# Performance work log

Measured on AMD Instinct MI355X. Metric: run time of the kernel, lower is better.

## Reference

```python
import jax, jax.numpy as jnp
import numpy as np

SAMPLE_POINTS = 1000
THRESH = 0.1
MAX_RATIO = 0.1
BIG = 1e9


def _sobel_boundary(mask):
    # mask: [B, H, W] -> boundary magnitude [B, H, W]
    kx = jnp.array([[-1, 0, 1], [-2, 0, 2], [-1, 0, 1]], jnp.float32).reshape(1, 1, 3, 3)
    ky = jnp.array([[-1, -2, -1], [0, 0, 0], [1, 2, 1]], jnp.float32).reshape(1, 1, 3, 3)
    x = mask[:, None, :, :]
    dn = ('NCHW', 'OIHW', 'NCHW')
    gx = jax.lax.conv_general_dilated(x, kx, (1, 1), [(1, 1), (1, 1)], dimension_numbers=dn)
    gy = jax.lax.conv_general_dilated(x, ky, (1, 1), [(1, 1), (1, 1)], dimension_numbers=dn)
    return jnp.sqrt(gx * gx + gy * gy + 1e-8)[:, 0]


def _extract_points(bmap, keys, H, W):
    # bmap: [B, H, W]. Returns points [B, P, 2] float and validity mask [B, P].
    # Torch version uses torch.where + randperm subsampling; here we pick a
    # uniformly-random subset of valid boundary pixels via noisy top_k
    # (fixed-shape, jit-compatible stream compaction).
    def one(bm, key):
        flat = bm.reshape(-1)
        valid = flat > THRESH
        noise = jax.random.uniform(key, flat.shape)
        score = valid.astype(jnp.float32) * 2.0 + noise  # valid in (2,3), invalid in (0,1)
        _, idx = jax.lax.top_k(score, SAMPLE_POINTS)
        pts = jnp.stack([(idx // W).astype(jnp.float32), (idx % W).astype(jnp.float32)], axis=-1)
        pvalid = valid[idx]
        has_any = valid.any()
        # empty-boundary fallback: single center point (like torch version)
        center = jnp.array([H // 2, W // 2], jnp.float32)
        pts = jnp.where(has_any, pts, jnp.broadcast_to(center, pts.shape))
        pvalid = jnp.where(has_any, pvalid, jnp.arange(SAMPLE_POINTS) == 0)
        return pts, pvalid

    return jax.vmap(one)(bmap, keys)


def _hausdorff(pp, pv, tp, tv, diag):
    # pp: [B,P,2], tp: [B,T,2]; masked symmetric Hausdorff per batch element.
    pp2 = jnp.sum(pp * pp, -1)  # [B,P]
    tp2 = jnp.sum(tp * tp, -1)  # [B,T]
    d2 = pp2[:, :, None] + tp2[:, None, :] - 2.0 * jnp.einsum('bpc,btc->bpt', pp, tp)
    D = jnp.sqrt(jnp.maximum(d2, 0.0))  # [B,P,T]
    min_p2t = jnp.min(jnp.where(tv[:, None, :], D, BIG), axis=2)  # [B,P]
    a = jnp.max(jnp.where(pv, min_p2t, -BIG), axis=1)  # [B]
    min_t2p = jnp.min(jnp.where(pv[:, :, None], D, BIG), axis=1)  # [B,T]
    b = jnp.max(jnp.where(tv, min_t2p, -BIG), axis=1)  # [B]
    hd = jnp.maximum(a, b) / diag
    return jnp.clip(hd, 0.0, MAX_RATIO)


def setup_inputs() -> dict:
    key = jax.random.key(0)
    k1, k2 = jax.random.split(key)
    B, H, W = 64, 512, 512
    pred_logits = jax.random.normal(k1, (B, H, W), dtype=jnp.float32)
    target = (jax.random.uniform(k2, (B, H, W)) > 0.5).astype(jnp.float32)
    return {"pred_logits": pred_logits, "target": target}


def reference(pred_logits, target):
    B, H, W = pred_logits.shape
    pred_probs = jax.nn.sigmoid(pred_logits)
    bmap_pred = _sobel_boundary(pred_probs)
    bmap_tgt = _sobel_boundary(target)
    keys = jax.random.split(jax.random.key(1), 2 * B)
    pp, pv = _extract_points(bmap_pred, keys[:B], H, W)
    tp, tv = _extract_points(bmap_tgt, keys[B:], H, W)
    diag = jnp.sqrt(jnp.float32(H * H + W * W))
    hd = _hausdorff(pp, pv, tp, tv, diag)  # [B]
    return jnp.mean(hd)
```

## Files before the change

kernel.cpp:

```cpp
#include <hip/hip_runtime.h>
#include <stdint.h>


#define HH 512
#define WW 512
#define NPIX (HH * WW)
#define NSEL 1000
#define SLICE_CAP 320
#define CUTM (253u << 14)
#define BITCUT ((((253u << 15) - 1u)) << 9)
#define ROWS_PER 32
#define K2_BS 1024

#if __has_builtin(__builtin_amdgcn_alignbit)
__device__ __forceinline__ uint32_t rotl32(uint32_t x, int r) {
  return __builtin_amdgcn_alignbit(x, x, (32 - r) & 31);
}
#else
__device__ __forceinline__ uint32_t rotl32(uint32_t x, int r) {
  return (x << r) | (x >> (32 - r));
}
#endif

template <int R>
__device__ __forceinline__ uint32_t rotlT(uint32_t x) {
  uint32_t d;
  asm("v_alignbit_b32 %0, %1, %1, %2" : "=v"(d) : "v"(x), "n"(32 - R));
  return d;
}

__device__ __forceinline__ void tf2x32(uint32_t k0, uint32_t k1,
                                       uint32_t c0, uint32_t c1,
                                       uint32_t& o0, uint32_t& o1) {
  uint32_t ks2 = k0 ^ k1 ^ 0x1BD11BDAu;
  uint32_t x0 = c0 + k0, x1 = c1 + k1;
#define TF_R(r) { x0 += x1; x1 = rotl32(x1, (r)); x1 ^= x0; }
  TF_R(13) TF_R(15) TF_R(26) TF_R(6)
  x0 += k1;  x1 += ks2 + 1u;
  TF_R(17) TF_R(29) TF_R(16) TF_R(24)
  x0 += ks2; x1 += k0 + 2u;
  TF_R(13) TF_R(15) TF_R(26) TF_R(6)
  x0 += k0;  x1 += k1 + 3u;
  TF_R(17) TF_R(29) TF_R(16) TF_R(24)
  x0 += k1;  x1 += ks2 + 4u;
  TF_R(13) TF_R(15) TF_R(26) TF_R(6)
  x0 += ks2; x1 += k0 + 5u;
#undef TF_R
  o0 = x0; o1 = x1;
}

__device__ __forceinline__ uint32_t m_from_bits(uint32_t bits) {
  float noise = __uint_as_float((bits >> 9) | 0x3F800000u) - 1.0f;
  float score = 2.0f + noise;
  return __float_as_uint(score) - 0x40000000u;
}

__device__ __forceinline__ uint32_t pixel_m(uint32_t k0, uint32_t k1, int p) {
  uint32_t b1, b2;
  tf2x32(k0, k1, 0u, (uint32_t)p, b1, b2);
  return m_from_bits(b1 ^ b2);
}

__device__ __forceinline__ float sigf(float x) { return 1.0f / (1.0f + __expf(-x)); }

__device__ __forceinline__ float ldval(const float* __restrict__ img, int r, int c, bool isPred) {
  if (r < 0 || r > HH - 1 || c < 0 || c > WW - 1) return 0.0f;
  float v = img[(size_t)r * WW + c];
  return isPred ? sigf(v) : v;
}

__device__ __forceinline__ uint32_t pack_pt(uint32_t p) {
  return ((p >> 9) << 16) | (p & 511u);
}

template <bool PRED>
__device__ __forceinline__ void sobel_body(const float* __restrict__ img, int b,
                                           int slice, int t,
                                           unsigned long long* stage, int* s_cn,
                                           int* s_cv) {
  const int lane = t & 63, w = t >> 6;
  const int rbase = slice * ROWS_PER + 8 * w;
  uint32_t k0, k1;
  tf2x32(0u, 1u, 0u, (uint32_t)b, k0, k1);
  k0 = __builtin_amdgcn_readfirstlane(k0);
  k1 = __builtin_amdgcn_readfirstlane(k1);
  const uint32_t ks2 = k0 ^ k1 ^ 0x1BD11BDAu;

  float P[10], Q[10], R[10];
  float4 na, nb;
  int cnt = 0;
  const uint32_t pbase = (uint32_t)((rbase << 9) + (lane << 3));

  auto issue = [&](int rn) {
    if ((unsigned)rn < (unsigned)HH) {
      const float* rp = img + ((size_t)rn << 9) + (lane << 3);
      na = *(const float4*)rp;
      nb = *(const float4*)(rp + 4);
    }
  };
  auto promote = [&](float (&vv)[10], int rn) {
    if ((unsigned)rn < (unsigned)HH) {
      float4 x = na, y = nb;
      if (PRED) {
        x.x = sigf(x.x); x.y = sigf(x.y); x.z = sigf(x.z); x.w = sigf(x.w);
        y.x = sigf(y.x); y.y = sigf(y.y); y.z = sigf(y.z); y.w = sigf(y.w);
      }
      vv[1] = x.x; vv[2] = x.y; vv[3] = x.z; vv[4] = x.w;
      vv[5] = y.x; vv[6] = y.y; vv[7] = y.z; vv[8] = y.w;
      float l = __shfl_up(y.w, 1);
      float r = __shfl_down(x.x, 1);
      vv[0] = (lane == 0) ? 0.0f : l;
      vv[9] = (lane == 63) ? 0.0f : r;
    } else {
#pragma unroll
      for (int i = 0; i < 10; ++i) vv[i] = 0.0f;
    }
  };

  issue(rbase - 1); promote(P, rbase - 1);
  issue(rbase);     promote(Q, rbase);
  issue(rbase + 1);

#pragma unroll 1
  for (int r = 0; r < 8; ++r) {
    promote(R, rbase + r + 1);
    if (r < 7) issue(rbase + r + 2);
    __builtin_amdgcn_sched_barrier(0);

    const uint32_t prow = pbase + ((uint32_t)r << 9);
    uint32_t X0[8], X1[8];
    const uint32_t pk = prow + k1;
    const uint32_t s0 = pk + k0;
#pragma unroll
    for (int j = 0; j < 8; ++j) {
      uint32_t x1i = pk + (uint32_t)j;
      X0[j] = s0 + (uint32_t)j;
      X1[j] = rotlT<13>(x1i) ^ X0[j];
    }
#define RND(rr)                                                         \
  _Pragma("unroll") for (int j = 0; j < 8; ++j) {                       \
    X0[j] += X1[j];                                                     \
    X1[j] = rotlT<(rr)>(X1[j]) ^ X0[j];                                 \
  }
#define INJ(ka, kb, i)                                                  \
  _Pragma("unroll") for (int j = 0; j < 8; ++j) {                       \
    X0[j] += (ka);                                                      \
    X1[j] += (kb) + (uint32_t)(i);                                      \
  }
    RND(15) RND(26) RND(6)  INJ(k1, ks2, 1)
    RND(17) RND(29) RND(16) RND(24) INJ(ks2, k0, 2)
    RND(13) RND(15) RND(26) RND(6)  INJ(k0, k1, 3)
    RND(17) RND(29) RND(16) RND(24) INJ(k1, ks2, 4)
    RND(13) RND(15) RND(26) RND(6)  INJ(ks2, k0, 5)
#undef RND
#undef INJ
    uint32_t bits[8];
#pragma unroll
    for (int j = 0; j < 8; ++j) bits[j] = X0[j] ^ X1[j];

    float da[10], e[10];
#pragma unroll
    for (int k = 0; k < 10; ++k) {
      da[k] = R[k] - P[k];
      e[k] = P[k] + 2.0f * Q[k] + R[k];
    }
    uint32_t candmask = 0;
#pragma unroll
    for (int j = 0; j < 8; ++j) {
      float gx = e[j + 2] - e[j];
      float gy = da[j] + 2.0f * da[j + 1] + da[j + 2];
      bool vld = (gx * gx + gy * gy + 1e-8f) > 0.01f;
      cnt += vld ? 1 : 0;
      candmask |= ((vld && bits[j] >= BITCUT) ? 1u : 0u) << j;
    }
    if (candmask) {
      int base = atomicAdd(s_cn, __popc(candmask));
      do {
        int j = __ffs(candmask) - 1;
        candmask &= candmask - 1;
        if (base < SLICE_CAP) {
          uint32_t m = m_from_bits(bits[j]);
          stage[base] = ((unsigned long long)m << 32) | (prow + (uint32_t)j);
        }
        ++base;
      } while (candmask);
    }
#pragma unroll
    for (int k = 0; k < 10; ++k) { P[k] = Q[k]; Q[k] = R[k]; }
  }
#pragma unroll
  for (int o = 32; o > 0; o >>= 1) cnt += __shfl_down(cnt, o);
  if (lane == 0) atomicAdd(s_cv, cnt);
}

__global__ __launch_bounds__(256, 4) void sobel_cand(
    const float* __restrict__ pred, const float* __restrict__ tgt,
    int2* __restrict__ g_scnt, unsigned long long* __restrict__ g_cand,
    uint32_t* __restrict__ g_hmax, int* __restrict__ g_done) {
  const int bid = blockIdx.x;
  const int b = bid >> 4, s = bid & 15;
  const int t = threadIdx.x;
  __shared__ unsigned long long stage[SLICE_CAP];
  __shared__ int s_cn, s_cv;
  if (t == 0) { s_cn = 0; s_cv = 0; }
  if (bid == 0) {
    if (t < 64) g_hmax[t] = 0u;
    if (t == 64) *g_done = 0;
  }
  __syncthreads();
  if (b < 64) sobel_body<true>(pred + (size_t)b * NPIX, b, s, t, stage, &s_cn, &s_cv);
  else        sobel_body<false>(tgt + (size_t)(b - 64) * NPIX, b, s, t, stage, &s_cn, &s_cv);
  __syncthreads();
  const int raw = s_cn;
  const int n = raw < SLICE_CAP ? raw : SLICE_CAP;
  for (int i = t; i < n; i += 256) g_cand[(size_t)bid * SLICE_CAP + i] = stage[i];
  if (t == 0) g_scnt[bid] = make_int2(s_cv, raw);
}

__global__ __launch_bounds__(K2_BS) void resolve_kernel(
    const float* __restrict__ pred, const float* __restrict__ tgt,
    const int2* __restrict__ g_scnt, unsigned long long* __restrict__ g_cand,
    uint32_t* __restrict__ g_pts, int* __restrict__ g_counts) {
  const int img = blockIdx.x;
  const int t = threadIdx.x;
  const int lane = t & 63;

  __shared__ unsigned long long cand_s[16 * SLICE_CAP];
  __shared__ int segc[16], segoff[17];
  __shared__ int s_scx[16], s_scy[16];
  __shared__ int s_info[4];
  __shared__ int ch[256];
  __shared__ int fh[1024];
  __shared__ int aux[256];
  __shared__ unsigned long long ties[256];
  __shared__ int s_pos, s_nt, s_T1, s_r1, s_T2, s_r2, s_n;

  if (t < 16) {
    int2 v = g_scnt[img * 16 + t];
    s_scx[t] = v.x; s_scy[t] = v.y;
    segc[t] = v.y < SLICE_CAP ? v.y : SLICE_CAP;
  }
  if (t == 0) { s_pos = 0; s_nt = 0; }
  __syncthreads();
  if (t == 0) {
    int cv = 0, hi = 0, ovf = 0, off = 0;
    for (int s = 0; s < 16; ++s) {
      cv += s_scx[s]; hi += s_scy[s];
      if (s_scy[s] > SLICE_CAP) ovf = 1;
      segoff[s] = off; off += segc[s];
    }
    segoff[16] = off;
    s_n = off;
    s_info[0] = cv; s_info[1] = hi; s_info[2] = ovf;
  }
  __syncthreads();
  const int cv = s_info[0];
  if (cv == 0) {
    if (t == 0) { g_pts[img * NSEL] = (256u << 16) | 256u; g_counts[img] = 1; }
    return;
  }
  const int need = cv < NSEL ? cv : NSEL;
  const bool slow = (s_info[2] != 0) || (s_info[1] < need);

  unsigned long long* C = g_cand + (size_t)img * 16 * SLICE_CAP;

  if (slow) {
    const bool isPred = img < 64;
    const float* im = isPred ? pred + (size_t)img * NPIX : tgt + (size_t)(img - 64) * NPIX;
    uint32_t k0, k1;
    tf2x32(0u, 1u, 0u, (uint32_t)img, k0, k1);
    if (t < 256) ch[t] = 0;
    __syncthreads();
    for (int p = t; p < NPIX; p += K2_BS) {
      int r = p >> 9, c = p & 511;
      float gx = (ldval(im, r - 1, c + 1, isPred) - ldval(im, r - 1, c - 1, isPred)) +
                 2.0f * (ldval(im, r, c + 1, isPred) - ldval(im, r, c - 1, isPred)) +
                 (ldval(im, r + 1, c + 1, isPred) - ldval(im, r + 1, c - 1, isPred));
      float gy = (ldval(im, r + 1, c - 1, isPred) - ldval(im, r - 1, c - 1, isPred)) +
                 2.0f * (ldval(im, r + 1, c, isPred) - ldval(im, r - 1, c, isPred)) +
                 (ldval(im, r + 1, c + 1, isPred) - ldval(im, r - 1, c + 1, isPred));
      if ((gx * gx + gy * gy + 1e-8f) > 0.01f) {
        uint32_t m = pixel_m(k0, k1, p);
        uint32_t cb = m >> 14; if (cb > 255u) cb = 255u;
        atomicAdd(&ch[cb], 1);
      }
    }
    __syncthreads();
    if (t < 256) aux[t] = ch[t];
    __syncthreads();
    for (int o = 1; o < 256; o <<= 1) {
      int v = 0;
      if (t < 256 && t + o < 256) v = aux[t + o];
      __syncthreads();
      if (t < 256) aux[t] += v;
      __syncthreads();
    }
    if (t < 256) {
      int nx = (t + 1 < 256) ? aux[t + 1] : 0;
      if (aux[t] >= need && nx < need) s_T1 = t;
    }
    __syncthreads();
    const uint32_t Tc = (uint32_t)s_T1;
    if (t == 0) s_info[3] = 0;
    __syncthreads();
    for (int p = t; p < NPIX; p += K2_BS) {
      int r = p >> 9, c = p & 511;
      float gx = (ldval(im, r - 1, c + 1, isPred) - ldval(im, r - 1, c - 1, isPred)) +
                 2.0f * (ldval(im, r, c + 1, isPred) - ldval(im, r, c - 1, isPred)) +
                 (ldval(im, r + 1, c + 1, isPred) - ldval(im, r + 1, c - 1, isPred));
      float gy = (ldval(im, r + 1, c - 1, isPred) - ldval(im, r - 1, c - 1, isPred)) +
                 2.0f * (ldval(im, r + 1, c, isPred) - ldval(im, r - 1, c, isPred)) +
                 (ldval(im, r + 1, c + 1, isPred) - ldval(im, r - 1, c + 1, isPred));
      if ((gx * gx + gy * gy + 1e-8f) > 0.01f) {
        uint32_t m = pixel_m(k0, k1, p);
        uint32_t cb = m >> 14; if (cb > 255u) cb = 255u;
        if (cb >= Tc) {
          int i = atomicAdd(&s_info[3], 1);
          if (i < 16 * SLICE_CAP) C[i] = ((unsigned long long)m << 32) | (uint32_t)p;
        }
      }
    }
    __syncthreads();
    if (t == 0) s_n = s_info[3] < 16 * SLICE_CAP ? s_info[3] : 16 * SLICE_CAP;
    __syncthreads();
  }

  {
    const int nn = s_n;
    if (slow) {
      for (int i = t; i < nn; i += K2_BS) cand_s[i] = C[i];
    } else {
      for (int i = t; i < 16 * SLICE_CAP; i += K2_BS) {
        int s = i / SLICE_CAP;
        int o = i - s * SLICE_CAP;
        if (o < segc[s]) cand_s[segoff[s] + o] = C[i];
      }
    }
  }
  if (t < 256) ch[t] = 0;
  fh[t] = 0;
  __syncthreads();
  const int n = s_n;

  if (!slow) {
    int l0 = 0, l1 = 0, l2 = 0;
    for (int i = t; i < n; i += K2_BS) {
      uint32_t cb = (uint32_t)(cand_s[i] >> 32) >> 14; if (cb > 255u) cb = 255u;
      if (cb == 253u) ++l0; else if (cb == 254u) ++l1; else ++l2;
    }
#pragma unroll
    for (int o = 32; o > 0; o >>= 1) {
      l0 += __shfl_down(l0, o); l1 += __shfl_down(l1, o); l2 += __shfl_down(l2, o);
    }
    if (lane == 0) {
      if (l0) atomicAdd(&ch[253], l0);
      if (l1) atomicAdd(&ch[254], l1);
      if (l2) atomicAdd(&ch[255], l2);
    }
  } else {
    for (int i = t; i < n; i += K2_BS) {
      uint32_t cb = (uint32_t)(cand_s[i] >> 32) >> 14; if (cb > 255u) cb = 255u;
      atomicAdd(&ch[cb], 1);
    }
  }
  __syncthreads();
  if (t < 256) aux[t] = ch[t];
  __syncthreads();
  for (int o = 1; o < 256; o <<= 1) {
    int v = 0;
    if (t < 256 && t + o < 256) v = aux[t + o];
    __syncthreads();
    if (t < 256) aux[t] += v;
    __syncthreads();
  }
  if (t < 256) {
    int nx = (t + 1 < 256) ? aux[t + 1] : 0;
    if (aux[t] >= need && nx < need) { s_T1 = t; s_r1 = need - nx; }
  }
  __syncthreads();
  const uint32_t T1 = (uint32_t)s_T1;
  const int r1 = s_r1;
  const uint32_t baseM = T1 << 14;

  for (int base = 0; base < n; base += K2_BS) {
    const int i = base + t;
    const bool in = i < n;
    unsigned long long e = in ? cand_s[i] : 0ull;
    uint32_t m = (uint32_t)(e >> 32), p = (uint32_t)e;
    uint32_t cb = m >> 14; if (cb > 255u) cb = 255u;
    bool emit = in && cb > T1;
    unsigned long long msk = __ballot(emit);
    if (msk) {
      int leader = __ffsll(msk) - 1;
      int bpos = 0;
      if (lane == leader) bpos = atomicAdd(&s_pos, __popcll(msk));
      bpos = __shfl(bpos, leader);
      if (emit)
        g_pts[img * NSEL + bpos + __popcll(msk & ((1ull << lane) - 1ull))] = pack_pt(p);
    }
    if (in && cb == T1) {
      uint32_t f = (m - baseM) >> 4; if (f > 1023u) f = 1023u;
      atomicAdd(&fh[f], 1);
    }
  }
  __syncthreads();
  for (int o = 1; o < 1024; o <<= 1) {
    int v = (t + o < 1024) ? fh[t + o] : 0;
    __syncthreads();
    fh[t] += v;
    __syncthreads();
  }
  {
    int nx = (t < 1023) ? fh[t + 1] : 0;
    if (fh[t] >= r1 && nx < r1) { s_T2 = t; s_r2 = r1 - nx; }
  }
  __syncthreads();
  const int T2 = s_T2, r2 = s_r2;

  for (int base = 0; base < n; base += K2_BS) {
    const int i = base + t;
    const bool in = i < n;
    unsigned long long e = in ? cand_s[i] : 0ull;
    uint32_t m = (uint32_t)(e >> 32), p = (uint32_t)e;
    uint32_t cb = m >> 14; if (cb > 255u) cb = 255u;
    uint32_t f = (m - baseM) >> 4; if (f > 1023u) f = 1023u;
    const bool isT1 = in && cb == T1;
    bool emit = isT1 && (int)f > T2;
    bool tie  = isT1 && (int)f == T2;
    unsigned long long msk = __ballot(emit);
    if (msk) {
      int leader = __ffsll(msk) - 1;
      int bpos = 0;
      if (lane == leader) bpos = atomicAdd(&s_pos, __popcll(msk));
      bpos = __shfl(bpos, leader);
      if (emit)
        g_pts[img * NSEL + bpos + __popcll(msk & ((1ull << lane) - 1ull))] = pack_pt(p);
    }
    unsigned long long mt = __ballot(tie);
    if (mt) {
      int leader = __ffsll(mt) - 1;
      int bpos = 0;
      if (lane == leader) bpos = atomicAdd(&s_nt, __popcll(mt));
      bpos = __shfl(bpos, leader);
      int idx = bpos + __popcll(mt & ((1ull << lane) - 1ull));
      if (tie && idx < 256) ties[idx] = e;
    }
  }
  __syncthreads();
  const int nt = s_nt < 256 ? s_nt : 256;
  for (int i = t; i < nt; i += K2_BS) {
    unsigned long long e = ties[i];
    uint32_t mi = (uint32_t)(e >> 32), pi = (uint32_t)e;
    int rank = 0;
    for (int j = 0; j < nt; ++j) {
      unsigned long long e2 = ties[j];
      uint32_t mj = (uint32_t)(e2 >> 32), pj = (uint32_t)e2;
      rank += (mj > mi) || (mj == mi && pj < pi);
    }
    if (rank < r2) {
      int pos = atomicAdd(&s_pos, 1);
      g_pts[img * NSEL + pos] = pack_pt(pi);
    }
  }
  __syncthreads();
  if (t == 0) g_counts[img] = s_pos;
}

__global__ __launch_bounds__(256) void haus_kernel(
    const uint32_t* __restrict__ g_pts, const int* __restrict__ g_counts,
    uint32_t* __restrict__ g_hmax, int* __restrict__ g_done,
    float* __restrict__ out) {
  const int bid = blockIdx.x;
  const int img = bid >> 3;
  const int dir = (bid >> 2) & 1;
  const int seg = bid & 3;
  const int t = threadIdx.x;
  const int iOwn = dir ? 64 + img : img;
  const int iOth = dir ? img : 64 + img;
  const int nOwn = g_counts[iOwn];
  const int nOth = g_counts[iOth];
  __shared__ float2 o[NSEL];
  __shared__ float red[256];
  __shared__ int s_ticket;
  for (int i = t; i < nOth; i += 256) {
    uint32_t v = g_pts[iOth * NSEL + i];
    o[i] = make_float2((float)(v >> 16), (float)(v & 0xFFFFu));
  }
  __syncthreads();
  float best = 0.0f;
  const int lo = seg * 250;
  const int hi = min(nOwn, lo + 250);
  for (int i = lo + t; i < hi; i += 256) {
    uint32_t v = g_pts[iOwn * NSEL + i];
    float pr = (float)(v >> 16), pc = (float)(v & 0xFFFFu);
    float mn0 = 3.4e38f, mn1 = 3.4e38f, mn2 = 3.4e38f, mn3 = 3.4e38f;
    int j = 0;
    for (; j + 3 < nOth; j += 4) {
      float dr0 = pr - o[j].x,     dc0 = pc - o[j].y;
      float dr1 = pr - o[j + 1].x, dc1 = pc - o[j + 1].y;
      float dr2 = pr - o[j + 2].x, dc2 = pc - o[j + 2].y;
      float dr3 = pr - o[j + 3].x, dc3 = pc - o[j + 3].y;
      mn0 = fminf(mn0, dr0 * dr0 + dc0 * dc0);
      mn1 = fminf(mn1, dr1 * dr1 + dc1 * dc1);
      mn2 = fminf(mn2, dr2 * dr2 + dc2 * dc2);
      mn3 = fminf(mn3, dr3 * dr3 + dc3 * dc3);
    }
    for (; j < nOth; ++j) {
      float dr = pr - o[j].x, dc = pc - o[j].y;
      mn0 = fminf(mn0, dr * dr + dc * dc);
    }
    float mn = fminf(fminf(mn0, mn1), fminf(mn2, mn3));
    best = fmaxf(best, mn);
  }
  red[t] = best;
  __syncthreads();
  for (int st = 128; st > 0; st >>= 1) {
    if (t < st) red[t] = fmaxf(red[t], red[t + st]);
    __syncthreads();
  }
  if (t == 0) {
    atomicMax(&g_hmax[img], __float_as_uint(red[0]));
    __threadfence();
    s_ticket = atomicAdd(g_done, 1);
  }
  __syncthreads();
  if (s_ticket == 511) {
    __threadfence();
    if (t < 64) {
      uint32_t u = atomicMax(&g_hmax[t], 0u);
      float diag = sqrtf((float)(HH * HH + WW * WW));
      float hd = sqrtf(fmaxf(__uint_as_float(u), 0.0f)) / diag;
      hd = fminf(fmaxf(hd, 0.0f), 0.1f);
      float s = hd;
      for (int o2 = 32; o2 > 0; o2 >>= 1) s += __shfl_down(s, o2);
      if (t == 0) out[0] = s * 0.015625f;
    }
  }
}

#define WS_SCNT   0u
#define WS_COUNTS 16384u
#define WS_HMAX   (WS_COUNTS + 512u)
#define WS_DONE   (WS_HMAX + 256u)
#define WS_PTS    (WS_HMAX + 2048u)
#define WS_CAND   (WS_PTS + 512000u)

extern "C" void kernel_launch(void* const* d_in, const int* in_sizes, int n_in,
                              void* d_out, int out_size, void* d_ws, size_t ws_size,
                              hipStream_t stream) {
  const float* pred = (const float*)d_in[0];
  const float* tgt = (const float*)d_in[1];
  float* out = (float*)d_out;
  char* ws = (char*)d_ws;
  int2* g_scnt = (int2*)(ws + WS_SCNT);
  int* g_counts = (int*)(ws + WS_COUNTS);
  uint32_t* g_hmax = (uint32_t*)(ws + WS_HMAX);
  int* g_done = (int*)(ws + WS_DONE);
  uint32_t* g_pts = (uint32_t*)(ws + WS_PTS);
  unsigned long long* g_cand = (unsigned long long*)(ws + WS_CAND);

  sobel_cand<<<2048, 256, 0, stream>>>(pred, tgt, g_scnt, g_cand, g_hmax, g_done);
  resolve_kernel<<<128, K2_BS, 0, stream>>>(pred, tgt, g_scnt, g_cand, g_pts, g_counts);
  haus_kernel<<<512, 256, 0, stream>>>(g_pts, g_counts, g_hmax, g_done, out);
}
```

Baseline: 233.4 us.

## Fuse sobel, resolve and Hausdorff kernels into one persistent-style kernel with flags

Merges the three launches into a single 2048-block kernel. Slice-0 blocks spin-wait on per-image counters, then do candidate resolution with 256 threads reading candidates straight from global memory. Blocks for slices 8-11 wait on per-image ready flags and compute the Hausdorff terms. This removes launch gaps and the end-of-kernel barriers, but adds spin-waits that can deadlock if dependent blocks are not co-resident, and makes resolution slower per image because it runs with 256 threads instead of 1024. A memset is added to clear the flags.

```diff
diff --git a/kernel.cpp b/kernel.cpp
--- a/kernel.cpp
+++ b/kernel.cpp
@@ -10,7 +10,6 @@
 #define CUTM (253u << 14)
 #define BITCUT ((((253u << 15) - 1u)) << 9)
 #define ROWS_PER 32
-#define K2_BS 1024
 
 #if __has_builtin(__builtin_amdgcn_alignbit)
 __device__ __forceinline__ uint32_t rotl32(uint32_t x, int r) {
@@ -193,356 +192,382 @@
   if (lane == 0) atomicAdd(s_cv, cnt);
 }
 
-__global__ __launch_bounds__(256, 4) void sobel_cand(
+__global__ __launch_bounds__(256, 4) void fused_kernel(
     const float* __restrict__ pred, const float* __restrict__ tgt,
     int2* __restrict__ g_scnt, unsigned long long* __restrict__ g_cand,
-    uint32_t* __restrict__ g_hmax, int* __restrict__ g_done) {
-  const int bid = blockIdx.x;
-  const int b = bid >> 4, s = bid & 15;
-  const int t = threadIdx.x;
-  __shared__ unsigned long long stage[SLICE_CAP];
-  __shared__ int s_cn, s_cv;
-  if (t == 0) { s_cn = 0; s_cv = 0; }
-  if (bid == 0) {
-    if (t < 64) g_hmax[t] = 0u;
-    if (t == 64) *g_done = 0;
-  }
-  __syncthreads();
-  if (b < 64) sobel_body<true>(pred + (size_t)b * NPIX, b, s, t, stage, &s_cn, &s_cv);
-  else        sobel_body<false>(tgt + (size_t)(b - 64) * NPIX, b, s, t, stage, &s_cn, &s_cv);
-  __syncthreads();
-  const int raw = s_cn;
-  const int n = raw < SLICE_CAP ? raw : SLICE_CAP;
-  for (int i = t; i < n; i += 256) g_cand[(size_t)bid * SLICE_CAP + i] = stage[i];
-  if (t == 0) g_scnt[bid] = make_int2(s_cv, raw);
-}
-
-__global__ __launch_bounds__(K2_BS) void resolve_kernel(
-    const float* __restrict__ pred, const float* __restrict__ tgt,
-    const int2* __restrict__ g_scnt, unsigned long long* __restrict__ g_cand,
-    uint32_t* __restrict__ g_pts, int* __restrict__ g_counts) {
-  const int img = blockIdx.x;
-  const int t = threadIdx.x;
-  const int lane = t & 63;
-
-  __shared__ unsigned long long cand_s[16 * SLICE_CAP];
-  __shared__ int segc[16], segoff[17];
-  __shared__ int s_scx[16], s_scy[16];
-  __shared__ int s_info[4];
-  __shared__ int ch[256];
-  __shared__ int fh[1024];
-  __shared__ int aux[256];
-  __shared__ unsigned long long ties[256];
-  __shared__ int s_pos, s_nt, s_T1, s_r1, s_T2, s_r2, s_n;
-
-  if (t < 16) {
-    int2 v = g_scnt[img * 16 + t];
-    s_scx[t] = v.x; s_scy[t] = v.y;
-    segc[t] = v.y < SLICE_CAP ? v.y : SLICE_CAP;
-  }
-  if (t == 0) { s_pos = 0; s_nt = 0; }
-  __syncthreads();
-  if (t == 0) {
-    int cv = 0, hi = 0, ovf = 0, off = 0;
-    for (int s = 0; s < 16; ++s) {
-      cv += s_scx[s]; hi += s_scy[s];
-      if (s_scy[s] > SLICE_CAP) ovf = 1;
-      segoff[s] = off; off += segc[s];
-    }
-    segoff[16] = off;
-    s_n = off;
-    s_info[0] = cv; s_info[1] = hi; s_info[2] = ovf;
-  }
-  __syncthreads();
-  const int cv = s_info[0];
-  if (cv == 0) {
-    if (t == 0) { g_pts[img * NSEL] = (256u << 16) | 256u; g_counts[img] = 1; }
-    return;
-  }
-  const int need = cv < NSEL ? cv : NSEL;
-  const bool slow = (s_info[2] != 0) || (s_info[1] < need);
-
-  unsigned long long* C = g_cand + (size_t)img * 16 * SLICE_CAP;
-
-  if (slow) {
-    const bool isPred = img < 64;
-    const float* im = isPred ? pred + (size_t)img * NPIX : tgt + (size_t)(img - 64) * NPIX;
-    uint32_t k0, k1;
-    tf2x32(0u, 1u, 0u, (uint32_t)img, k0, k1);
-    if (t < 256) ch[t] = 0;
-    __syncthreads();
-    for (int p = t; p < NPIX; p += K2_BS) {
-      int r = p >> 9, c = p & 511;
-      float gx = (ldval(im, r - 1, c + 1, isPred) - ldval(im, r - 1, c - 1, isPred)) +
-                 2.0f * (ldval(im, r, c + 1, isPred) - ldval(im, r, c - 1, isPred)) +
-                 (ldval(im, r + 1, c + 1, isPred) - ldval(im, r + 1, c - 1, isPred));
-      float gy = (ldval(im, r + 1, c - 1, isPred) - ldval(im, r - 1, c - 1, isPred)) +
-                 2.0f * (ldval(im, r + 1, c, isPred) - ldval(im, r - 1, c, isPred)) +
-                 (ldval(im, r + 1, c + 1, isPred) - ldval(im, r - 1, c + 1, isPred));
-      if ((gx * gx + gy * gy + 1e-8f) > 0.01f) {
-        uint32_t m = pixel_m(k0, k1, p);
-        uint32_t cb = m >> 14; if (cb > 255u) cb = 255u;
-        atomicAdd(&ch[cb], 1);
-      }
-    }
-    __syncthreads();
-    if (t < 256) aux[t] = ch[t];
-    __syncthreads();
-    for (int o = 1; o < 256; o <<= 1) {
-      int v = 0;
-      if (t < 256 && t + o < 256) v = aux[t + o];
-      __syncthreads();
-      if (t < 256) aux[t] += v;
-      __syncthreads();
-    }
-    if (t < 256) {
-      int nx = (t + 1 < 256) ? aux[t + 1] : 0;
-      if (aux[t] >= need && nx < need) s_T1 = t;
-    }
-    __syncthreads();
-    const uint32_t Tc = (uint32_t)s_T1;
-    if (t == 0) s_info[3] = 0;
-    __syncthreads();
-    for (int p = t; p < NPIX; p += K2_BS) {
-      int r = p >> 9, c = p & 511;
-      float gx = (ldval(im, r - 1, c + 1, isPred) - ldval(im, r - 1, c - 1, isPred)) +
-                 2.0f * (ldval(im, r, c + 1, isPred) - ldval(im, r, c - 1, isPred)) +
-                 (ldval(im, r + 1, c + 1, isPred) - ldval(im, r + 1, c - 1, isPred));
-      float gy = (ldval(im, r + 1, c - 1, isPred) - ldval(im, r - 1, c - 1, isPred)) +
-                 2.0f * (ldval(im, r + 1, c, isPred) - ldval(im, r - 1, c, isPred)) +
-                 (ldval(im, r + 1, c + 1, isPred) - ldval(im, r - 1, c + 1, isPred));
-      if ((gx * gx + gy * gy + 1e-8f) > 0.01f) {
-        uint32_t m = pixel_m(k0, k1, p);
-        uint32_t cb = m >> 14; if (cb > 255u) cb = 255u;
-        if (cb >= Tc) {
-          int i = atomicAdd(&s_info[3], 1);
-          if (i < 16 * SLICE_CAP) C[i] = ((unsigned long long)m << 32) | (uint32_t)p;
-        }
-      }
-    }
-    __syncthreads();
-    if (t == 0) s_n = s_info[3] < 16 * SLICE_CAP ? s_info[3] : 16 * SLICE_CAP;
-    __syncthreads();
-  }
-
-  {
-    const int nn = s_n;
-    if (slow) {
-      for (int i = t; i < nn; i += K2_BS) cand_s[i] = C[i];
-    } else {
-      for (int i = t; i < 16 * SLICE_CAP; i += K2_BS) {
-        int s = i / SLICE_CAP;
-        int o = i - s * SLICE_CAP;
-        if (o < segc[s]) cand_s[segoff[s] + o] = C[i];
-      }
-    }
-  }
-  if (t < 256) ch[t] = 0;
-  fh[t] = 0;
-  __syncthreads();
-  const int n = s_n;
-
-  if (!slow) {
-    int l0 = 0, l1 = 0, l2 = 0;
-    for (int i = t; i < n; i += K2_BS) {
-      uint32_t cb = (uint32_t)(cand_s[i] >> 32) >> 14; if (cb > 255u) cb = 255u;
-      if (cb == 253u) ++l0; else if (cb == 254u) ++l1; else ++l2;
-    }
-#pragma unroll
-    for (int o = 32; o > 0; o >>= 1) {
-      l0 += __shfl_down(l0, o); l1 += __shfl_down(l1, o); l2 += __shfl_down(l2, o);
-    }
-    if (lane == 0) {
-      if (l0) atomicAdd(&ch[253], l0);
-      if (l1) atomicAdd(&ch[254], l1);
-      if (l2) atomicAdd(&ch[255], l2);
-    }
-  } else {
-    for (int i = t; i < n; i += K2_BS) {
-      uint32_t cb = (uint32_t)(cand_s[i] >> 32) >> 14; if (cb > 255u) cb = 255u;
-      atomicAdd(&ch[cb], 1);
-    }
-  }
-  __syncthreads();
-  if (t < 256) aux[t] = ch[t];
-  __syncthreads();
-  for (int o = 1; o < 256; o <<= 1) {
-    int v = 0;
-    if (t < 256 && t + o < 256) v = aux[t + o];
-    __syncthreads();
-    if (t < 256) aux[t] += v;
-    __syncthreads();
-  }
-  if (t < 256) {
-    int nx = (t + 1 < 256) ? aux[t + 1] : 0;
-    if (aux[t] >= need && nx < need) { s_T1 = t; s_r1 = need - nx; }
-  }
-  __syncthreads();
-  const uint32_t T1 = (uint32_t)s_T1;
-  const int r1 = s_r1;
-  const uint32_t baseM = T1 << 14;
-
-  for (int base = 0; base < n; base += K2_BS) {
-    const int i = base + t;
-    const bool in = i < n;
-    unsigned long long e = in ? cand_s[i] : 0ull;
-    uint32_t m = (uint32_t)(e >> 32), p = (uint32_t)e;
-    uint32_t cb = m >> 14; if (cb > 255u) cb = 255u;
-    bool emit = in && cb > T1;
-    unsigned long long msk = __ballot(emit);
-    if (msk) {
-      int leader = __ffsll(msk) - 1;
-      int bpos = 0;
-      if (lane == leader) bpos = atomicAdd(&s_pos, __popcll(msk));
-      bpos = __shfl(bpos, leader);
-      if (emit)
-        g_pts[img * NSEL + bpos + __popcll(msk & ((1ull << lane) - 1ull))] = pack_pt(p);
-    }
-    if (in && cb == T1) {
-      uint32_t f = (m - baseM) >> 4; if (f > 1023u) f = 1023u;
-      atomicAdd(&fh[f], 1);
-    }
-  }
-  __syncthreads();
-  for (int o = 1; o < 1024; o <<= 1) {
-    int v = (t + o < 1024) ? fh[t + o] : 0;
-    __syncthreads();
-    fh[t] += v;
-    __syncthreads();
-  }
-  {
-    int nx = (t < 1023) ? fh[t + 1] : 0;
-    if (fh[t] >= r1 && nx < r1) { s_T2 = t; s_r2 = r1 - nx; }
-  }
-  __syncthreads();
-  const int T2 = s_T2, r2 = s_r2;
-
-  for (int base = 0; base < n; base += K2_BS) {
-    const int i = base + t;
-    const bool in = i < n;
-    unsigned long long e = in ? cand_s[i] : 0ull;
-    uint32_t m = (uint32_t)(e >> 32), p = (uint32_t)e;
-    uint32_t cb = m >> 14; if (cb > 255u) cb = 255u;
-    uint32_t f = (m - baseM) >> 4; if (f > 1023u) f = 1023u;
-    const bool isT1 = in && cb == T1;
-    bool emit = isT1 && (int)f > T2;
-    bool tie  = isT1 && (int)f == T2;
-    unsigned long long msk = __ballot(emit);
-    if (msk) {
-      int leader = __ffsll(msk) - 1;
-      int bpos = 0;
-      if (lane == leader) bpos = atomicAdd(&s_pos, __popcll(msk));
-      bpos = __shfl(bpos, leader);
-      if (emit)
-        g_pts[img * NSEL + bpos + __popcll(msk & ((1ull << lane) - 1ull))] = pack_pt(p);
-    }
-    unsigned long long mt = __ballot(tie);
-    if (mt) {
-      int leader = __ffsll(mt) - 1;
-      int bpos = 0;
-      if (lane == leader) bpos = atomicAdd(&s_nt, __popcll(mt));
-      bpos = __shfl(bpos, leader);
-      int idx = bpos + __popcll(mt & ((1ull << lane) - 1ull));
-      if (tie && idx < 256) ties[idx] = e;
-    }
-  }
-  __syncthreads();
-  const int nt = s_nt < 256 ? s_nt : 256;
-  for (int i = t; i < nt; i += K2_BS) {
-    unsigned long long e = ties[i];
-    uint32_t mi = (uint32_t)(e >> 32), pi = (uint32_t)e;
-    int rank = 0;
-    for (int j = 0; j < nt; ++j) {
-      unsigned long long e2 = ties[j];
-      uint32_t mj = (uint32_t)(e2 >> 32), pj = (uint32_t)e2;
-      rank += (mj > mi) || (mj == mi && pj < pi);
-    }
-    if (rank < r2) {
-      int pos = atomicAdd(&s_pos, 1);
-      g_pts[img * NSEL + pos] = pack_pt(pi);
-    }
-  }
-  __syncthreads();
-  if (t == 0) g_counts[img] = s_pos;
-}
-
-__global__ __launch_bounds__(256) void haus_kernel(
-    const uint32_t* __restrict__ g_pts, const int* __restrict__ g_counts,
+    uint32_t* __restrict__ g_pts, int* __restrict__ g_counts,
+    int* __restrict__ done_img, int* __restrict__ rdone,
     uint32_t* __restrict__ g_hmax, int* __restrict__ g_done,
     float* __restrict__ out) {
   const int bid = blockIdx.x;
-  const int img = bid >> 3;
-  const int dir = (bid >> 2) & 1;
-  const int seg = bid & 3;
+  const int side = bid >> 4, slice = bid & 15;
   const int t = threadIdx.x;
-  const int iOwn = dir ? 64 + img : img;
-  const int iOth = dir ? img : 64 + img;
-  const int nOwn = g_counts[iOwn];
-  const int nOth = g_counts[iOth];
-  __shared__ float2 o[NSEL];
+  const int lane = t & 63;
+
+  __shared__ unsigned long long stage[SLICE_CAP];
+  __shared__ int s_cn, s_cv;
+  __shared__ int segc[16], s_scx[16], s_scy[16];
+  __shared__ int s_info[4];
+  __shared__ int ch[256], fh[1024], aux[256];
+  __shared__ unsigned long long ties[256];
+  __shared__ int s_pos, s_nt, s_T1, s_r1, s_T2, s_r2;
+  __shared__ float2 opts[NSEL];
   __shared__ float red[256];
-  __shared__ int s_ticket;
-  for (int i = t; i < nOth; i += 256) {
-    uint32_t v = g_pts[iOth * NSEL + i];
-    o[i] = make_float2((float)(v >> 16), (float)(v & 0xFFFFu));
+  __shared__ int s_tk;
+
+  if (t == 0) { s_cn = 0; s_cv = 0; }
+  __syncthreads();
+  if (side < 64)
+    sobel_body<true>(pred + (size_t)side * NPIX, side, slice, t, stage, &s_cn, &s_cv);
+  else
+    sobel_body<false>(tgt + (size_t)(side - 64) * NPIX, side, slice, t, stage, &s_cn, &s_cv);
+  __syncthreads();
+  {
+    const int raw = s_cn;
+    const int n = raw < SLICE_CAP ? raw : SLICE_CAP;
+    for (int i = t; i < n; i += 256) g_cand[(size_t)bid * SLICE_CAP + i] = stage[i];
+    if (t == 0) g_scnt[bid] = make_int2(s_cv, raw);
   }
   __syncthreads();
-  float best = 0.0f;
-  const int lo = seg * 250;
-  const int hi = min(nOwn, lo + 250);
-  for (int i = lo + t; i < hi; i += 256) {
-    uint32_t v = g_pts[iOwn * NSEL + i];
-    float pr = (float)(v >> 16), pc = (float)(v & 0xFFFFu);
-    float mn0 = 3.4e38f, mn1 = 3.4e38f, mn2 = 3.4e38f, mn3 = 3.4e38f;
-    int j = 0;
-    for (; j + 3 < nOth; j += 4) {
-      float dr0 = pr - o[j].x,     dc0 = pc - o[j].y;
-      float dr1 = pr - o[j + 1].x, dc1 = pc - o[j + 1].y;
-      float dr2 = pr - o[j + 2].x, dc2 = pc - o[j + 2].y;
-      float dr3 = pr - o[j + 3].x, dc3 = pc - o[j + 3].y;
-      mn0 = fminf(mn0, dr0 * dr0 + dc0 * dc0);
-      mn1 = fminf(mn1, dr1 * dr1 + dc1 * dc1);
-      mn2 = fminf(mn2, dr2 * dr2 + dc2 * dc2);
-      mn3 = fminf(mn3, dr3 * dr3 + dc3 * dc3);
-    }
-    for (; j < nOth; ++j) {
-      float dr = pr - o[j].x, dc = pc - o[j].y;
-      mn0 = fminf(mn0, dr * dr + dc * dc);
-    }
-    float mn = fminf(fminf(mn0, mn1), fminf(mn2, mn3));
-    best = fmaxf(best, mn);
+  if (t == 0) { __threadfence(); atomicAdd(&done_img[side], 1); }
+
+  if (slice == 0) {
+    const int img = side;
+    if (t == 0) {
+      while (atomicAdd(&done_img[img], 0) < 16) __builtin_amdgcn_s_sleep(8);
+      __threadfence();
+    }
+    __syncthreads();
+
+    if (t < 16) {
+      int2 v = g_scnt[img * 16 + t];
+      s_scx[t] = v.x; s_scy[t] = v.y;
+      segc[t] = v.y < SLICE_CAP ? v.y : SLICE_CAP;
+    }
+    if (t == 0) { s_pos = 0; s_nt = 0; }
+    __syncthreads();
+    if (t == 0) {
+      int cv = 0, hi = 0, ovf = 0;
+      for (int s = 0; s < 16; ++s) {
+        cv += s_scx[s]; hi += s_scy[s];
+        if (s_scy[s] > SLICE_CAP) ovf = 1;
+      }
+      s_info[0] = cv; s_info[1] = hi; s_info[2] = ovf;
+    }
+    __syncthreads();
+    const int cv = s_info[0];
+    if (cv == 0) {
+      if (t == 0) { g_pts[img * NSEL] = (256u << 16) | 256u; g_counts[img] = 1; }
+    } else {
+      const int need = cv < NSEL ? cv : NSEL;
+      const bool slow = (s_info[2] != 0) || (s_info[1] < need);
+      unsigned long long* C = g_cand + (size_t)img * 16 * SLICE_CAP;
+
+      if (slow) {
+        const bool isPred = img < 64;
+        const float* im = isPred ? pred + (size_t)img * NPIX
+                                 : tgt + (size_t)(img - 64) * NPIX;
+        uint32_t k0, k1;
+        tf2x32(0u, 1u, 0u, (uint32_t)img, k0, k1);
+        ch[t] = 0;
+        __syncthreads();
+        for (int p = t; p < NPIX; p += 256) {
+          int r = p >> 9, c = p & 511;
+          float gx = (ldval(im, r - 1, c + 1, isPred) - ldval(im, r - 1, c - 1, isPred)) +
+                     2.0f * (ldval(im, r, c + 1, isPred) - ldval(im, r, c - 1, isPred)) +
+                     (ldval(im, r + 1, c + 1, isPred) - ldval(im, r + 1, c - 1, isPred));
+          float gy = (ldval(im, r + 1, c - 1, isPred) - ldval(im, r - 1, c - 1, isPred)) +
+                     2.0f * (ldval(im, r + 1, c, isPred) - ldval(im, r - 1, c, isPred)) +
+                     (ldval(im, r + 1, c + 1, isPred) - ldval(im, r - 1, c + 1, isPred));
+          if ((gx * gx + gy * gy + 1e-8f) > 0.01f) {
+            uint32_t m = pixel_m(k0, k1, p);
+            uint32_t cb = m >> 14; if (cb > 255u) cb = 255u;
+            atomicAdd(&ch[cb], 1);
+          }
+        }
+        __syncthreads();
+        {
+          aux[t] = ch[t];
+          __syncthreads();
+          for (int o = 1; o < 256; o <<= 1) {
+            int v = (t + o < 256) ? aux[t + o] : 0;
+            __syncthreads();
+            aux[t] += v;
+            __syncthreads();
+          }
+          int nx = (t + 1 < 256) ? aux[t + 1] : 0;
+          if (aux[t] >= need && nx < need) s_T1 = t;
+          __syncthreads();
+        }
+        const uint32_t Tc = (uint32_t)s_T1;
+        if (t == 0) s_info[3] = 0;
+        __syncthreads();
+        for (int p = t; p < NPIX; p += 256) {
+          int r = p >> 9, c = p & 511;
+          float gx = (ldval(im, r - 1, c + 1, isPred) - ldval(im, r - 1, c - 1, isPred)) +
+                     2.0f * (ldval(im, r, c + 1, isPred) - ldval(im, r, c - 1, isPred)) +
+                     (ldval(im, r + 1, c + 1, isPred) - ldval(im, r + 1, c - 1, isPred));
+          float gy = (ldval(im, r + 1, c - 1, isPred) - ldval(im, r - 1, c - 1, isPred)) +
+                     2.0f * (ldval(im, r + 1, c, isPred) - ldval(im, r - 1, c, isPred)) +
+                     (ldval(im, r + 1, c + 1, isPred) - ldval(im, r - 1, c + 1, isPred));
+          if ((gx * gx + gy * gy + 1e-8f) > 0.01f) {
+            uint32_t m = pixel_m(k0, k1, p);
+            uint32_t cb = m >> 14; if (cb > 255u) cb = 255u;
+            if (cb >= Tc) {
+              int i = atomicAdd(&s_info[3], 1);
+              if (i < 16 * SLICE_CAP) C[i] = ((unsigned long long)m << 32) | (uint32_t)p;
+            }
+          }
+        }
+        __syncthreads();
+        if (t == 0) {
+          int nc = s_info[3] < 16 * SLICE_CAP ? s_info[3] : 16 * SLICE_CAP;
+          segc[0] = nc;
+          for (int s = 1; s < 16; ++s) segc[s] = 0;
+        }
+        __syncthreads();
+      }
+
+      ch[t] = 0;
+      for (int i = t; i < 1024; i += 256) fh[i] = 0;
+      __syncthreads();
+      if (!slow) {
+        int l0 = 0, l1 = 0, l2 = 0;
+        for (int s = 0; s < 16; ++s) {
+          const unsigned long long* sp = C + (size_t)s * SLICE_CAP;
+          for (int i = t; i < segc[s]; i += 256) {
+            uint32_t cb = (uint32_t)(sp[i] >> 32) >> 14;
+            if (cb >= 255u) ++l2; else if (cb == 254u) ++l1; else ++l0;
+          }
+        }
+#pragma unroll
+        for (int o = 32; o > 0; o >>= 1) {
+          l0 += __shfl_down(l0, o); l1 += __shfl_down(l1, o); l2 += __shfl_down(l2, o);
+        }
+        if (lane == 0) {
+          if (l0) atomicAdd(&ch[253], l0);
+          if (l1) atomicAdd(&ch[254], l1);
+          if (l2) atomicAdd(&ch[255], l2);
+        }
+        __syncthreads();
+        if (t == 0) {
+          int s5 = ch[255], s4 = ch[254] + s5;
+          if (s5 >= need)      { s_T1 = 255; s_r1 = need; }
+          else if (s4 >= need) { s_T1 = 254; s_r1 = need - s5; }
+          else                 { s_T1 = 253; s_r1 = need - s4; }
+        }
+        __syncthreads();
+      } else {
+        for (int s = 0; s < 16; ++s) {
+          const unsigned long long* sp = C + (size_t)s * SLICE_CAP;
+          for (int i = t; i < segc[s]; i += 256) {
+            uint32_t cb = (uint32_t)(sp[i] >> 32) >> 14; if (cb > 255u) cb = 255u;
+            atomicAdd(&ch[cb], 1);
+          }
+        }
+        __syncthreads();
+        aux[t] = ch[t];
+        __syncthreads();
+        for (int o = 1; o < 256; o <<= 1) {
+          int v = (t + o < 256) ? aux[t + o] : 0;
+          __syncthreads();
+          aux[t] += v;
+          __syncthreads();
+        }
+        int nx = (t + 1 < 256) ? aux[t + 1] : 0;
+        if (aux[t] >= need && nx < need) { s_T1 = t; s_r1 = need - nx; }
+        __syncthreads();
+      }
+      const uint32_t T1 = (uint32_t)s_T1;
+      const int r1 = s_r1;
+      const uint32_t baseM = T1 << 14;
+
+      for (int s = 0; s < 16; ++s) {
+        const unsigned long long* sp = C + (size_t)s * SLICE_CAP;
+        const int sn = segc[s];
+        for (int i0 = 0; i0 < sn; i0 += 256) {
+          const int i = i0 + t;
+          const bool in = i < sn;
+          unsigned long long e = in ? sp[i] : 0ull;
+          uint32_t m = (uint32_t)(e >> 32), p = (uint32_t)e;
+          uint32_t cb = m >> 14; if (cb > 255u) cb = 255u;
+          bool emit = in && cb > T1;
+          unsigned long long msk = __ballot(emit);
+          if (msk) {
+            int leader = __ffsll((unsigned long long)msk) - 1;
+            int bpos = 0;
+            if (lane == leader) bpos = atomicAdd(&s_pos, __popcll(msk));
+            bpos = __shfl(bpos, leader);
+            if (emit)
+              g_pts[img * NSEL + bpos + __popcll(msk & ((1ull << lane) - 1ull))] = pack_pt(p);
+          }
+          if (in && cb == T1) {
+            uint32_t f = (m - baseM) >> 4; if (f > 1023u) f = 1023u;
+            atomicAdd(&fh[f], 1);
+          }
+        }
+      }
+      __syncthreads();
+      {
+        int base4 = 4 * t, sv = 0;
+        for (int j = 3; j >= 0; --j) { sv += fh[base4 + j]; fh[base4 + j] = sv; }
+        aux[t] = sv;
+        __syncthreads();
+        for (int o = 1; o < 256; o <<= 1) {
+          int v = (t + o < 256) ? aux[t + o] : 0;
+          __syncthreads();
+          aux[t] += v;
+          __syncthreads();
+        }
+        int add = (t < 255) ? aux[t + 1] : 0;
+        for (int j = 0; j < 4; ++j) fh[base4 + j] += add;
+        __syncthreads();
+        for (int j = 0; j < 4; ++j) {
+          int idx = base4 + j;
+          int sfx = fh[idx];
+          int nx2 = (idx < 1023) ? fh[idx + 1] : 0;
+          if (sfx >= r1 && nx2 < r1) { s_T2 = idx; s_r2 = r1 - nx2; }
+        }
+        __syncthreads();
+      }
+      const int T2 = s_T2, r2 = s_r2;
+
+      for (int s = 0; s < 16; ++s) {
+        const unsigned long long* sp = C + (size_t)s * SLICE_CAP;
+        const int sn = segc[s];
+        for (int i0 = 0; i0 < sn; i0 += 256) {
+          const int i = i0 + t;
+          const bool in = i < sn;
+          unsigned long long e = in ? sp[i] : 0ull;
+          uint32_t m = (uint32_t)(e >> 32), p = (uint32_t)e;
+          uint32_t cb = m >> 14; if (cb > 255u) cb = 255u;
+          uint32_t f = (m - baseM) >> 4; if (f > 1023u) f = 1023u;
+          const bool isT1 = in && cb == T1;
+          bool emit = isT1 && (int)f > T2;
+          bool tie  = isT1 && (int)f == T2;
+          unsigned long long msk = __ballot(emit);
+          if (msk) {
+            int leader = __ffsll((unsigned long long)msk) - 1;
+            int bpos = 0;
+            if (lane == leader) bpos = atomicAdd(&s_pos, __popcll(msk));
+            bpos = __shfl(bpos, leader);
+            if (emit)
+              g_pts[img * NSEL + bpos + __popcll(msk & ((1ull << lane) - 1ull))] = pack_pt(p);
+          }
+          unsigned long long mt = __ballot(tie);
+          if (mt) {
+            int leader = __ffsll((unsigned long long)mt) - 1;
+            int bpos = 0;
+            if (lane == leader) bpos = atomicAdd(&s_nt, __popcll(mt));
+            bpos = __shfl(bpos, leader);
+            int idx = bpos + __popcll(mt & ((1ull << lane) - 1ull));
+            if (tie && idx < 256) ties[idx] = e;
+          }
+        }
+      }
+      __syncthreads();
+      const int nt = s_nt < 256 ? s_nt : 256;
+      for (int i = t; i < nt; i += 256) {
+        unsigned long long e = ties[i];
+        uint32_t mi = (uint32_t)(e >> 32), pi = (uint32_t)e;
+        int rank = 0;
+        for (int j = 0; j < nt; ++j) {
+          unsigned long long e2 = ties[j];
+          uint32_t mj = (uint32_t)(e2 >> 32), pj = (uint32_t)e2;
+          rank += (mj > mi) || (mj == mi && pj < pi);
+        }
+        if (rank < r2) {
+          int pos = atomicAdd(&s_pos, 1);
+          g_pts[img * NSEL + pos] = pack_pt(pi);
+        }
+      }
+      __syncthreads();
+      if (t == 0) g_counts[img] = s_pos;
+    }
+    __syncthreads();
+    if (t == 0) { __threadfence(); atomicExch(&rdone[img], 1); }
   }
-  red[t] = best;
-  __syncthreads();
-  for (int st = 128; st > 0; st >>= 1) {
-    if (t < st) red[t] = fmaxf(red[t], red[t + st]);
-    __syncthreads();
-  }
-  if (t == 0) {
-    atomicMax(&g_hmax[img], __float_as_uint(red[0]));
-    __threadfence();
-    s_ticket = atomicAdd(g_done, 1);
-  }
-  __syncthreads();
-  if (s_ticket == 511) {
-    __threadfence();
-    if (t < 64) {
-      uint32_t u = atomicMax(&g_hmax[t], 0u);
-      float diag = sqrtf((float)(HH * HH + WW * WW));
-      float hd = sqrtf(fmaxf(__uint_as_float(u), 0.0f)) / diag;
-      hd = fminf(fmaxf(hd, 0.0f), 0.1f);
-      float s = hd;
-      for (int o2 = 32; o2 > 0; o2 >>= 1) s += __shfl_down(s, o2);
-      if (t == 0) out[0] = s * 0.015625f;
+
+  if (slice >= 8 && slice < 12) {
+    const int h = side * 4 + (slice - 8);
+    const int img = h >> 3;
+    const int dir = (h >> 2) & 1;
+    const int seg = h & 3;
+    const int iOwn = dir ? 64 + img : img;
+    const int iOth = dir ? img : 64 + img;
+    if (t == 0) {
+      while (atomicAdd(&rdone[iOwn], 0) == 0) __builtin_amdgcn_s_sleep(8);
+      while (atomicAdd(&rdone[iOth], 0) == 0) __builtin_amdgcn_s_sleep(8);
+      __threadfence();
+    }
+    __syncthreads();
+    const int nOwn = g_counts[iOwn];
+    const int nOth = g_counts[iOth];
+    for (int i = t; i < nOth; i += 256) {
+      uint32_t v = g_pts[iOth * NSEL + i];
+      opts[i] = make_float2((float)(v >> 16), (float)(v & 0xFFFFu));
+    }
+    __syncthreads();
+    float best = 0.0f;
+    const int lo = seg * 250;
+    const int hi = min(nOwn, lo + 250);
+    for (int i = lo + t; i < hi; i += 256) {
+      uint32_t v = g_pts[iOwn * NSEL + i];
+      float pr = (float)(v >> 16), pc = (float)(v & 0xFFFFu);
+      float mn0 = 3.4e38f, mn1 = 3.4e38f, mn2 = 3.4e38f, mn3 = 3.4e38f;
+      int j = 0;
+      for (; j + 3 < nOth; j += 4) {
+        float dr0 = pr - opts[j].x,     dc0 = pc - opts[j].y;
+        float dr1 = pr - opts[j + 1].x, dc1 = pc - opts[j + 1].y;
+        float dr2 = pr - opts[j + 2].x, dc2 = pc - opts[j + 2].y;
+        float dr3 = pr - opts[j + 3].x, dc3 = pc - opts[j + 3].y;
+        mn0 = fminf(mn0, dr0 * dr0 + dc0 * dc0);
+        mn1 = fminf(mn1, dr1 * dr1 + dc1 * dc1);
+        mn2 = fminf(mn2, dr2 * dr2 + dc2 * dc2);
+        mn3 = fminf(mn3, dr3 * dr3 + dc3 * dc3);
+      }
+      for (; j < nOth; ++j) {
+        float dr = pr - opts[j].x, dc = pc - opts[j].y;
+        mn0 = fminf(mn0, dr * dr + dc * dc);
+      }
+      float mn = fminf(fminf(mn0, mn1), fminf(mn2, mn3));
+      best = fmaxf(best, mn);
+    }
+    red[t] = best;
+    __syncthreads();
+    for (int st = 128; st > 0; st >>= 1) {
+      if (t < st) red[t] = fmaxf(red[t], red[t + st]);
+      __syncthreads();
+    }
+    if (t == 0) {
+      atomicMax(&g_hmax[img], __float_as_uint(red[0]));
+      __threadfence();
+      s_tk = atomicAdd(g_done, 1);
+    }
+    __syncthreads();
+    if (s_tk == 511) {
+      __threadfence();
+      if (t < 64) {
+        uint32_t u = atomicMax(&g_hmax[t], 0u);
+        float diag = sqrtf((float)(HH * HH + WW * WW));
+        float hd = sqrtf(fmaxf(__uint_as_float(u), 0.0f)) / diag;
+        hd = fminf(fmaxf(hd, 0.0f), 0.1f);
+        float s = hd;
+        for (int o2 = 32; o2 > 0; o2 >>= 1) s += __shfl_down(s, o2);
+        if (t == 0) out[0] = s * 0.015625f;
+      }
     }
   }
 }
 
 #define WS_SCNT   0u
 #define WS_COUNTS 16384u
-#define WS_HMAX   (WS_COUNTS + 512u)
-#define WS_DONE   (WS_HMAX + 256u)
-#define WS_PTS    (WS_HMAX + 2048u)
+#define WS_FLAGS  16896u
+#define WS_DONEIMG (WS_FLAGS)
+#define WS_RDONE  (WS_FLAGS + 512u)
+#define WS_HMAX   (WS_FLAGS + 1024u)
+#define WS_DONE   (WS_FLAGS + 1280u)
+#define WS_PTS    (WS_FLAGS + 1536u)
 #define WS_CAND   (WS_PTS + 512000u)
 
 extern "C" void kernel_launch(void* const* d_in, const int* in_sizes, int n_in,
@@ -554,12 +579,15 @@
   char* ws = (char*)d_ws;
   int2* g_scnt = (int2*)(ws + WS_SCNT);
   int* g_counts = (int*)(ws + WS_COUNTS);
+  int* done_img = (int*)(ws + WS_DONEIMG);
+  int* rdone = (int*)(ws + WS_RDONE);
   uint32_t* g_hmax = (uint32_t*)(ws + WS_HMAX);
   int* g_done = (int*)(ws + WS_DONE);
   uint32_t* g_pts = (uint32_t*)(ws + WS_PTS);
   unsigned long long* g_cand = (unsigned long long*)(ws + WS_CAND);
 
-  sobel_cand<<<2048, 256, 0, stream>>>(pred, tgt, g_scnt, g_cand, g_hmax, g_done);
-  resolve_kernel<<<128, K2_BS, 0, stream>>>(pred, tgt, g_scnt, g_cand, g_pts, g_counts);
-  haus_kernel<<<512, 256, 0, stream>>>(g_pts, g_counts, g_hmax, g_done, out);
-}
+  hipMemsetAsync(ws + WS_FLAGS, 0, 1536, stream);
+  fused_kernel<<<2048, 256, 0, stream>>>(pred, tgt, g_scnt, g_cand, g_pts,
+                                         g_counts, done_img, rdone, g_hmax,
+                                         g_done, out);
+}
```

Result: slower. 467.2 us (+100.2%).
